# Kernel optimization log

Hardware: AMD Instinct MI355X
Metric: run time of the kernel (lower is better)

## Reference

```python
import jax, jax.numpy as jnp
import numpy as np

B, F, E = 16384, 50, 64

def setup_inputs() -> dict:
    key = jax.random.key(0)
    k1, k2, k3, k4 = jax.random.split(key, 4)
    g = jax.random.uniform(k1, (B, F, F), dtype=jnp.float32)
    h = jax.random.normal(k2, (B, F, E), dtype=jnp.float32)
    W_in = jax.random.normal(k3, (F, E, E), dtype=jnp.float32) * (2.0 / (E + E)) ** 0.5
    W_out = jax.random.normal(k4, (F, E, E), dtype=jnp.float32) * (2.0 / (E + E)) ** 0.5
    bias_p = jnp.zeros((E,), dtype=jnp.float32)
    return {"g": g, "h": h, "W_in": W_in, "W_out": W_out, "bias_p": bias_p}

def reference(g, h, W_in, W_out, bias_p):
    # per-field transform: [F,E,E] x [B,F,E] -> [B,F,E]
    h_out = jnp.einsum('fij,bfj->bfi', W_out, h)
    # graph aggregation over fields: [B,F,F] x [B,F,E] -> [B,F,E]
    aggr = jnp.einsum('bfg,bge->bfe', g, h_out)
    # per-field input transform + bias
    a = jnp.einsum('fij,bfj->bfi', W_in, aggr) + bias_p
    return a
```

## Files before the change

kernel.cpp:

```cpp
#include <hip/hip_runtime.h>


static constexpr int Bz  = 16384;
static constexpr int Ff  = 50;
static constexpr int Ee  = 64;
static constexpr int BT  = 128;
static constexpr int LDW = 68;
static constexpr int GP  = 56;

__device__ __forceinline__ void fma4(float4& a, float s, const float4& v) {
    a.x += s * v.x; a.y += s * v.y; a.z += s * v.z; a.w += s * v.w;
}

__global__ __launch_bounds__(256, 3)
void field_gemm(const float* __restrict__ src, float* __restrict__ dst,
                const float* __restrict__ W, const float* __restrict__ bias) {
    __shared__ float W_lds[Ee * LDW];
    __shared__ float h_lds[BT * LDW];
    const int f  = blockIdx.y;
    const int b0 = blockIdx.x * BT;
    const int t  = threadIdx.x;

    const float* Wf = W + f * Ee * Ee;
#pragma unroll
    for (int k = 0; k < 16; ++k) {
        int idx = k * 256 + t;
        W_lds[(idx >> 6) * LDW + (idx & 63)] = Wf[idx];
    }
#pragma unroll
    for (int k = 0; k < (BT * Ee) / 256; ++k) {
        int idx = k * 256 + t;
        int bb = idx >> 6, j = idx & 63;
        h_lds[bb * LDW + j] = src[(b0 + bb) * (Ff * Ee) + f * Ee + j];
    }
    __syncthreads();

    const int ti = t & 15;
    const int tb = t >> 4;
    float acc[4][8];
#pragma unroll
    for (int ii = 0; ii < 4; ++ii)
#pragma unroll
        for (int kb = 0; kb < 8; ++kb) acc[ii][kb] = 0.f;

#pragma unroll 2
    for (int j0 = 0; j0 < Ee; j0 += 4) {
        float4 w4[4], h4[8];
#pragma unroll
        for (int ii = 0; ii < 4; ++ii)
            w4[ii] = *(const float4*)&W_lds[(ti + ii * 16) * LDW + j0];
#pragma unroll
        for (int kb = 0; kb < 8; ++kb)
            h4[kb] = *(const float4*)&h_lds[(tb + kb * 16) * LDW + j0];
#pragma unroll
        for (int ii = 0; ii < 4; ++ii)
#pragma unroll
            for (int kb = 0; kb < 8; ++kb) {
                acc[ii][kb] += w4[ii].x * h4[kb].x;
                acc[ii][kb] += w4[ii].y * h4[kb].y;
                acc[ii][kb] += w4[ii].z * h4[kb].z;
                acc[ii][kb] += w4[ii].w * h4[kb].w;
            }
    }

#pragma unroll
    for (int ii = 0; ii < 4; ++ii) {
        int i = ti + ii * 16;
        float bv = bias ? bias[i] : 0.0f;
#pragma unroll
        for (int kb = 0; kb < 8; ++kb) {
            int bb = tb + kb * 16;
            dst[(b0 + bb) * (Ff * Ee) + f * Ee + i] = acc[ii][kb] + bv;
        }
    }
}

__global__ __launch_bounds__(256)
void aggr_inplace(const float* __restrict__ g, float* __restrict__ ho) {
    __shared__ float ho_lds[GP * LDW];
    __shared__ float g_lds[Ff * GP];
    const int b = blockIdx.x;
    const int t = threadIdx.x;
    const float* gb = g + (size_t)b * (Ff * Ff);
    float*       hb = ho + (size_t)b * (Ff * Ee);

#pragma unroll
    for (int k = 0; k < 13; ++k) {
        int idx = k * 256 + t;
        if (idx < Ff * Ee)
            ho_lds[(idx >> 6) * LDW + (idx & 63)] = hb[idx];
    }
#pragma unroll
    for (int k = 0; k < 2; ++k) {
        int q = k * 256 + t;
        if (q < (GP - Ff) * Ee)
            ho_lds[(Ff + (q >> 6)) * LDW + (q & 63)] = 0.f;
    }
#pragma unroll
    for (int k = 0; k < 11; ++k) {
        int idx = k * 256 + t;
        if (idx < Ff * GP) {
            int ff = idx / GP, gg = idx - ff * GP;
            g_lds[idx] = (gg < Ff) ? gb[ff * Ff + gg] : 0.f;
        }
    }
    __syncthreads();

    const int te = t & 15;
    const int tf = t >> 4;
    float4 acc[4];
#pragma unroll
    for (int q = 0; q < 4; ++q) acc[q] = make_float4(0.f, 0.f, 0.f, 0.f);

#pragma unroll 2
    for (int g0 = 0; g0 < GP; g0 += 8) {
        float4 ho4[8];
#pragma unroll
        for (int q = 0; q < 8; ++q)
            ho4[q] = *(const float4*)&ho_lds[(g0 + q) * LDW + te * 4];
#pragma unroll
        for (int kf = 0; kf < 4; ++kf) {
            int fR = tf + kf * 16;
            if (fR < Ff) {
                float4 ga  = *(const float4*)&g_lds[fR * GP + g0];
                float4 gb4 = *(const float4*)&g_lds[fR * GP + g0 + 4];
                fma4(acc[kf], ga.x,  ho4[0]);
                fma4(acc[kf], ga.y,  ho4[1]);
                fma4(acc[kf], ga.z,  ho4[2]);
                fma4(acc[kf], ga.w,  ho4[3]);
                fma4(acc[kf], gb4.x, ho4[4]);
                fma4(acc[kf], gb4.y, ho4[5]);
                fma4(acc[kf], gb4.z, ho4[6]);
                fma4(acc[kf], gb4.w, ho4[7]);
            }
        }
    }

#pragma unroll
    for (int kf = 0; kf < 4; ++kf) {
        int fR = tf + kf * 16;
        if (fR < Ff)
            *(float4*)&hb[fR * Ee + te * 4] = acc[kf];
    }
}

extern "C" void kernel_launch(void* const* d_in, const int* in_sizes, int n_in,
                              void* d_out, int out_size, void* d_ws, size_t ws_size,
                              hipStream_t stream) {
    const float* g     = (const float*)d_in[0];
    const float* h     = (const float*)d_in[1];
    const float* W_in  = (const float*)d_in[2];
    const float* W_out = (const float*)d_in[3];
    const float* bias  = (const float*)d_in[4];
    float* out = (float*)d_out;

    dim3 grid1(Bz / BT, Ff);
    field_gemm<<<grid1, 256, 0, stream>>>(h, out, W_out, nullptr);
    aggr_inplace<<<Bz, 256, 0, stream>>>(g, out);
    field_gemm<<<grid1, 256, 0, stream>>>(out, out, W_in, bias);
}
```

Baseline: 694.5 us.

## Retile field GEMM and graph aggregation to 128-thread blocks with larger per-thread tiles

The field GEMM now runs with 128 threads per block, and each thread computes an 8x8 output tile instead of 4x8. Its global-to-LDS loads are vectorised with float4. The aggregation kernel now gives one wavefront to each batch element, packing two batches per block. It uses unpadded LDS layouts, float4 loads of g and h, and a 7-field by 8-element register tile per lane. The aim is more register reuse per LDS read and fewer LDS instructions, at the cost of higher register pressure and possible LDS bank conflicts from the unpadded and float2-strided access.

```diff
diff --git a/kernel.cpp b/kernel.cpp
--- a/kernel.cpp
+++ b/kernel.cpp
@@ -6,13 +6,12 @@
 static constexpr int Ee  = 64;
 static constexpr int BT  = 128;
 static constexpr int LDW = 68;
-static constexpr int GP  = 56;
 
 __device__ __forceinline__ void fma4(float4& a, float s, const float4& v) {
     a.x += s * v.x; a.y += s * v.y; a.z += s * v.z; a.w += s * v.w;
 }
 
-__global__ __launch_bounds__(256, 3)
+__global__ __launch_bounds__(128, 2)
 void field_gemm(const float* __restrict__ src, float* __restrict__ dst,
                 const float* __restrict__ W, const float* __restrict__ bias) {
     __shared__ float W_lds[Ee * LDW];
@@ -21,39 +20,41 @@
     const int b0 = blockIdx.x * BT;
     const int t  = threadIdx.x;
 
-    const float* Wf = W + f * Ee * Ee;
+    const float4* Wf4 = (const float4*)(W + f * Ee * Ee);
+#pragma unroll
+    for (int k = 0; k < 8; ++k) {
+        int q = k * 128 + t;
+        *(float4*)&W_lds[(q >> 4) * LDW + (q & 15) * 4] = Wf4[q];
+    }
+    const float4* s4 = (const float4*)src;
 #pragma unroll
     for (int k = 0; k < 16; ++k) {
-        int idx = k * 256 + t;
-        W_lds[(idx >> 6) * LDW + (idx & 63)] = Wf[idx];
-    }
-#pragma unroll
-    for (int k = 0; k < (BT * Ee) / 256; ++k) {
-        int idx = k * 256 + t;
-        int bb = idx >> 6, j = idx & 63;
-        h_lds[bb * LDW + j] = src[(b0 + bb) * (Ff * Ee) + f * Ee + j];
+        int q = k * 128 + t;
+        int r = q >> 4;
+        *(float4*)&h_lds[r * LDW + (q & 15) * 4] =
+            s4[(b0 + r) * (Ff * Ee / 4) + f * 16 + (q & 15)];
     }
     __syncthreads();
 
-    const int ti = t & 15;
-    const int tb = t >> 4;
-    float acc[4][8];
+    const int ti = t & 7;
+    const int tb = t >> 3;
+    float acc[8][8];
 #pragma unroll
-    for (int ii = 0; ii < 4; ++ii)
+    for (int ii = 0; ii < 8; ++ii)
 #pragma unroll
         for (int kb = 0; kb < 8; ++kb) acc[ii][kb] = 0.f;
 
 #pragma unroll 2
     for (int j0 = 0; j0 < Ee; j0 += 4) {
-        float4 w4[4], h4[8];
+        float4 w4[8], h4[8];
 #pragma unroll
-        for (int ii = 0; ii < 4; ++ii)
-            w4[ii] = *(const float4*)&W_lds[(ti + ii * 16) * LDW + j0];
+        for (int ii = 0; ii < 8; ++ii)
+            w4[ii] = *(const float4*)&W_lds[(ti + 8 * ii) * LDW + j0];
 #pragma unroll
         for (int kb = 0; kb < 8; ++kb)
-            h4[kb] = *(const float4*)&h_lds[(tb + kb * 16) * LDW + j0];
+            h4[kb] = *(const float4*)&h_lds[(tb + 16 * kb) * LDW + j0];
 #pragma unroll
-        for (int ii = 0; ii < 4; ++ii)
+        for (int ii = 0; ii < 8; ++ii)
 #pragma unroll
             for (int kb = 0; kb < 8; ++kb) {
                 acc[ii][kb] += w4[ii].x * h4[kb].x;
@@ -64,83 +65,86 @@
     }
 
 #pragma unroll
-    for (int ii = 0; ii < 4; ++ii) {
-        int i = ti + ii * 16;
-        float bv = bias ? bias[i] : 0.0f;
+    for (int ii = 0; ii < 8; ++ii) {
+        const int i  = ti + 8 * ii;
+        const float bv = bias ? bias[i] : 0.0f;
 #pragma unroll
         for (int kb = 0; kb < 8; ++kb) {
-            int bb = tb + kb * 16;
+            const int bb = tb + 16 * kb;
             dst[(b0 + bb) * (Ff * Ee) + f * Ee + i] = acc[ii][kb] + bv;
         }
     }
 }
 
-__global__ __launch_bounds__(256)
+static constexpr int HOP = 52 * Ee;
+static constexpr int GPD = 2560;
+static constexpr int WRG = HOP + GPD;
+
+__global__ __launch_bounds__(128, 2)
 void aggr_inplace(const float* __restrict__ g, float* __restrict__ ho) {
-    __shared__ float ho_lds[GP * LDW];
-    __shared__ float g_lds[Ff * GP];
-    const int b = blockIdx.x;
-    const int t = threadIdx.x;
-    const float* gb = g + (size_t)b * (Ff * Ff);
-    float*       hb = ho + (size_t)b * (Ff * Ee);
+    __shared__ float lds[2 * WRG];
+    const int t    = threadIdx.x;
+    const int wid  = t >> 6;
+    const int lane = t & 63;
+    const int b    = blockIdx.x * 2 + wid;
+    float* ho_sh = &lds[wid * WRG];
+    float* g_sh  = ho_sh + HOP;
 
+    const float4* hosrc = (const float4*)(ho + (size_t)b * (Ff * Ee));
+    const float4* gsrc  = (const float4*)(g  + (size_t)b * (Ff * Ff));
 #pragma unroll
     for (int k = 0; k < 13; ++k) {
-        int idx = k * 256 + t;
-        if (idx < Ff * Ee)
-            ho_lds[(idx >> 6) * LDW + (idx & 63)] = hb[idx];
+        int q = k * 64 + lane;
+        if (q < Ff * Ee / 4) *(float4*)&ho_sh[q * 4] = hosrc[q];
     }
 #pragma unroll
-    for (int k = 0; k < 2; ++k) {
-        int q = k * 256 + t;
-        if (q < (GP - Ff) * Ee)
-            ho_lds[(Ff + (q >> 6)) * LDW + (q & 63)] = 0.f;
+    for (int k = 0; k < 10; ++k) {
+        int q = k * 64 + lane;
+        if (q < (Ff * Ff + 3) / 4) *(float4*)&g_sh[q * 4] = gsrc[q];
     }
-#pragma unroll
-    for (int k = 0; k < 11; ++k) {
-        int idx = k * 256 + t;
-        if (idx < Ff * GP) {
-            int ff = idx / GP, gg = idx - ff * GP;
-            g_lds[idx] = (gg < Ff) ? gb[ff * Ff + gg] : 0.f;
-        }
-    }
+    *(float2*)&ho_sh[Ff * Ee + lane * 2] = make_float2(0.f, 0.f);
+    if (lane < 30) *(float2*)&g_sh[Ff * Ff + lane * 2] = make_float2(0.f, 0.f);
     __syncthreads();
 
-    const int te = t & 15;
-    const int tf = t >> 4;
-    float4 acc[4];
+    const int te = lane & 7;
+    const int tf = lane >> 3;
+    const int e0 = te * 8;
+    float4 acc[7][2];
 #pragma unroll
-    for (int q = 0; q < 4; ++q) acc[q] = make_float4(0.f, 0.f, 0.f, 0.f);
+    for (int k = 0; k < 7; ++k) {
+        acc[k][0] = make_float4(0.f, 0.f, 0.f, 0.f);
+        acc[k][1] = make_float4(0.f, 0.f, 0.f, 0.f);
+    }
 
 #pragma unroll 2
-    for (int g0 = 0; g0 < GP; g0 += 8) {
-        float4 ho4[8];
+    for (int g0 = 0; g0 < 52; g0 += 4) {
+        float4 ho4[4][2];
 #pragma unroll
-        for (int q = 0; q < 8; ++q)
-            ho4[q] = *(const float4*)&ho_lds[(g0 + q) * LDW + te * 4];
+        for (int q = 0; q < 4; ++q) {
+            ho4[q][0] = *(const float4*)&ho_sh[(g0 + q) * Ee + e0];
+            ho4[q][1] = *(const float4*)&ho_sh[(g0 + q) * Ee + e0 + 4];
+        }
 #pragma unroll
-        for (int kf = 0; kf < 4; ++kf) {
-            int fR = tf + kf * 16;
-            if (fR < Ff) {
-                float4 ga  = *(const float4*)&g_lds[fR * GP + g0];
-                float4 gb4 = *(const float4*)&g_lds[fR * GP + g0 + 4];
-                fma4(acc[kf], ga.x,  ho4[0]);
-                fma4(acc[kf], ga.y,  ho4[1]);
-                fma4(acc[kf], ga.z,  ho4[2]);
-                fma4(acc[kf], ga.w,  ho4[3]);
-                fma4(acc[kf], gb4.x, ho4[4]);
-                fma4(acc[kf], gb4.y, ho4[5]);
-                fma4(acc[kf], gb4.z, ho4[6]);
-                fma4(acc[kf], gb4.w, ho4[7]);
-            }
+        for (int k = 0; k < 7; ++k) {
+            int fi = tf * 7 + k;
+            fi = (fi < Ff) ? fi : (Ff - 1);
+            const float2 ga = *(const float2*)&g_sh[fi * Ff + g0];
+            const float2 gb = *(const float2*)&g_sh[fi * Ff + g0 + 2];
+            fma4(acc[k][0], ga.x, ho4[0][0]); fma4(acc[k][1], ga.x, ho4[0][1]);
+            fma4(acc[k][0], ga.y, ho4[1][0]); fma4(acc[k][1], ga.y, ho4[1][1]);
+            fma4(acc[k][0], gb.x, ho4[2][0]); fma4(acc[k][1], gb.x, ho4[2][1]);
+            fma4(acc[k][0], gb.y, ho4[3][0]); fma4(acc[k][1], gb.y, ho4[3][1]);
         }
     }
 
+    float* hb = ho + (size_t)b * (Ff * Ee);
 #pragma unroll
-    for (int kf = 0; kf < 4; ++kf) {
-        int fR = tf + kf * 16;
-        if (fR < Ff)
-            *(float4*)&hb[fR * Ee + te * 4] = acc[kf];
+    for (int k = 0; k < 7; ++k) {
+        const int fi = tf * 7 + k;
+        if (fi < Ff) {
+            *(float4*)&hb[fi * Ee + e0]     = acc[k][0];
+            *(float4*)&hb[fi * Ee + e0 + 4] = acc[k][1];
+        }
     }
 }
 
@@ -155,7 +159,7 @@
     float* out = (float*)d_out;
 
     dim3 grid1(Bz / BT, Ff);
-    field_gemm<<<grid1, 256, 0, stream>>>(h, out, W_out, nullptr);
-    aggr_inplace<<<Bz, 256, 0, stream>>>(g, out);
-    field_gemm<<<grid1, 256, 0, stream>>>(out, out, W_in, bias);
+    field_gemm<<<grid1, 128, 0, stream>>>(h, out, W_out, nullptr);
+    aggr_inplace<<<Bz / 2, 128, 0, stream>>>(g, out);
+    field_gemm<<<grid1, 128, 0, stream>>>(out, out, W_in, bias);
 }
```

After: 674.8 us. 2.8% less time.
